# Kernel optimization log

Measured on AMD Instinct MI355X. Metric: run time of the kernel, lower is better.

## Reference

```python
import jax, jax.numpy as jnp
import numpy as np

TOP_K = 2

def setup_inputs() -> dict:
    key = jax.random.key(0)
    k1, k2, k3, k4 = jax.random.split(key, 4)
    T, H, I, E = 8192, 2048, 4096, 8
    s = 0.02
    return {
        "hidden_states": jax.random.normal(k1, (T, H), dtype=jnp.float32),
        "router_w": jax.random.normal(k2, (E, H), dtype=jnp.float32) * s,
        "ws": jax.random.normal(k3, (E, 2 * I, H), dtype=jnp.float32) * s,  # [gate; up]
        "w2s": jax.random.normal(k4, (E, H, I), dtype=jnp.float32) * s,
    }

def reference(hidden_states, router_w, ws, w2s):
    # Router gating: softmax over experts, top-k, NO renormalization
    logits = hidden_states @ router_w.T              # [T, E]
    probs = jax.nn.softmax(logits, axis=-1)
    topv, topi = jax.lax.top_k(probs, TOP_K)         # [T, K]
    T, E = probs.shape
    I = w2s.shape[2]
    # Dense routing-weight matrix [T, E]; top_k indices are unique per token
    w = jnp.zeros_like(probs).at[jnp.arange(T)[:, None], topi].set(topv)
    out = jnp.zeros_like(hidden_states)
    for e in range(E):  # fixed small expert loop; avoids [T,E,2I] blowup
        gate = hidden_states @ ws[e, :I].T           # [T, I]
        up = hidden_states @ ws[e, I:].T             # [T, I]
        h = jax.nn.silu(gate) * up                   # SwiGLU
        out = out + w[:, e:e + 1] * (h @ w2s[e].T)   # combine
    return out
```

## Files before the change

### kernel.cpp

```cpp
#include <hip/hip_runtime.h>
#include <cstdint>
#include <cstddef>

#define T_TOK 8192
#define HDIM  2048
#define IDIM  4096
#define NEXP  8
#define MAXT  72

typedef __bf16 bf16x8 __attribute__((ext_vector_type(8)));
typedef float  f32x4  __attribute__((ext_vector_type(4)));

#define BARRIER() __builtin_amdgcn_s_barrier()
#define VMW(n)    do { asm volatile("s_waitcnt vmcnt(" #n ")" ::: "memory"); } while (0)
#define PRIO1()   __builtin_amdgcn_s_setprio(1)
#define PRIO0()   __builtin_amdgcn_s_setprio(0)

__device__ __forceinline__ unsigned short f2bf(float f) {
    union { float f; unsigned u; } v; v.f = f;
    unsigned r = v.u + 0x7FFFu + ((v.u >> 16) & 1u);
    return (unsigned short)(r >> 16);
}

__device__ __forceinline__ void gload16(const void* g, void* l) {
    __builtin_amdgcn_global_load_lds((__attribute__((address_space(1))) void*)g,
                                     (__attribute__((address_space(3))) void*)l,
                                     16, 0, 0);
}

__global__ __launch_bounds__(256) void router_k(const float* __restrict__ hs,
                                                const float* __restrict__ rw,
                                                float* __restrict__ wgt,
                                                int* __restrict__ counts,
                                                int* __restrict__ lists,
                                                unsigned short* __restrict__ hs_bf) {
    int gid  = blockIdx.x * 256 + threadIdx.x;
    int tok  = gid >> 6;
    int lane = threadIdx.x & 63;
    const float* x = hs + (size_t)tok * HDIM;
    unsigned short* xb = hs_bf + (size_t)tok * HDIM;

    float acc[NEXP];
#pragma unroll
    for (int e = 0; e < NEXP; ++e) acc[e] = 0.f;
    for (int h = lane; h < HDIM; h += 64) {
        float xv = x[h];
        xb[h] = f2bf(xv);
#pragma unroll
        for (int e = 0; e < NEXP; ++e) acc[e] = fmaf(xv, rw[e * HDIM + h], acc[e]);
    }
#pragma unroll
    for (int off = 32; off > 0; off >>= 1) {
#pragma unroll
        for (int e = 0; e < NEXP; ++e) acc[e] += __shfl_xor(acc[e], off, 64);
    }
    if (lane == 0) {
        float m = acc[0];
#pragma unroll
        for (int e = 1; e < NEXP; ++e) m = fmaxf(m, acc[e]);
        float p[NEXP]; float s = 0.f;
#pragma unroll
        for (int e = 0; e < NEXP; ++e) { p[e] = expf(acc[e] - m); s += p[e]; }
        float inv = 1.f / s;
        int i1 = 0;
#pragma unroll
        for (int e = 1; e < NEXP; ++e) if (acc[e] > acc[i1]) i1 = e;
        int i2 = -1;
#pragma unroll
        for (int e = 0; e < NEXP; ++e) if (e != i1 && (i2 < 0 || acc[e] > acc[i2])) i2 = e;
#pragma unroll
        for (int e = 0; e < NEXP; ++e)
            wgt[(size_t)tok * NEXP + e] = (e == i1 || e == i2) ? p[e] * inv : 0.f;
        int p1 = atomicAdd(&counts[i1], 1);
        lists[i1 * T_TOK + p1] = tok;
        int p2 = atomicAdd(&counts[i2], 1);
        lists[i2 * T_TOK + p2] = (1 << 16) | tok;
    }
}

__global__ void plan_k(const int* __restrict__ counts, int* __restrict__ offs,
                       int* __restrict__ desc, int* __restrict__ ntiles) {
    if (threadIdx.x == 0 && blockIdx.x == 0) {
        int off = 0, n = 0;
        for (int e = 0; e < NEXP; ++e) {
            offs[e] = off;
            int nt = (counts[e] + 255) >> 8;
            for (int t = 0; t < nt; ++t) desc[n++] = (e << 16) | t;
            off += nt * 256;
        }
        *ntiles = n;
    }
}

__global__ __launch_bounds__(256) void cvt_k(const float* __restrict__ in,
                                             unsigned short* __restrict__ out, long n4) {
    long i      = (long)blockIdx.x * 256 + threadIdx.x;
    long stride = (long)gridDim.x * 256;
    const float4* in4 = (const float4*)in;
    ushort4* out4 = (ushort4*)out;
    for (long j = i; j < n4; j += stride) {
        float4 v = in4[j];
        ushort4 o;
        o.x = f2bf(v.x); o.y = f2bf(v.y); o.z = f2bf(v.z); o.w = f2bf(v.w);
        out4[j] = o;
    }
}

__global__ __launch_bounds__(512, 2) void gemm1_k(const unsigned short* __restrict__ A,
                                                  const unsigned short* __restrict__ Wall,
                                                  unsigned short* __restrict__ Hout,
                                                  const int* __restrict__ lists,
                                                  const int* __restrict__ counts,
                                                  const int* __restrict__ offs,
                                                  const int* __restrict__ desc,
                                                  const int* __restrict__ ntiles) {
    const int slot = blockIdx.y;
    if (slot >= *ntiles) return;
    const int dsc = desc[slot];
    const int e = dsc >> 16, tt = dsc & 0xFFFF;
    const int cnt = counts[e];
    const int t0 = tt * 256;
    const int* list = lists + e * T_TOK;
    const unsigned short* W = Wall + (size_t)e * 2 * IDIM * HDIM;
    const int hbase = offs[e];
    const int n0 = blockIdx.x * 128;

    extern __shared__ __align__(16) char lds[];

    const int tid  = threadIdx.x;
    const int lane = tid & 63;
    const int wid  = tid >> 6;
    const int wr   = wid >> 2;
    const int wc   = wid & 3;

    const int prow = tid >> 3;
    const int pcol = (tid & 7) * 16;
    const int lcol = (pcol ^ ((prow & 7) << 4)) >> 1;
    unsigned aoff[4];
#pragma unroll
    for (int i = 0; i < 4; ++i) {
        int g = t0 + i * 64 + prow;
        int tok = list[(g < cnt) ? g : t0] & 0xFFFF;
        aoff[i] = (unsigned)tok * HDIM + lcol;
    }
    unsigned goff[2], uoff[2];
#pragma unroll
    for (int i = 0; i < 2; ++i) {
        goff[i] = (unsigned)(n0 + i * 64 + prow) * HDIM + lcol;
        uoff[i] = (unsigned)(IDIM + n0 + i * 64 + prow) * HDIM + lcol;
    }
    const int dst = tid * 16;

#define SG_AH0(b, t) do { unsigned k0_ = (unsigned)((t) & 31) * 64;      \
    gload16(A + aoff[0] + k0_, lds + (b) * 32768 + dst);                 \
    gload16(A + aoff[1] + k0_, lds + (b) * 32768 + 8192 + dst); } while (0)
#define SG_AH1(b, t) do { unsigned k0_ = (unsigned)((t) & 31) * 64;      \
    gload16(A + aoff[2] + k0_, lds + (b) * 32768 + 16384 + dst);         \
    gload16(A + aoff[3] + k0_, lds + (b) * 32768 + 24576 + dst); } while (0)
#define SG_G(b, t) do { unsigned k0_ = (unsigned)((t) & 31) * 64;        \
    gload16(W + goff[0] + k0_, lds + 65536 + (b) * 16384 + dst);         \
    gload16(W + goff[1] + k0_, lds + 65536 + (b) * 16384 + 8192 + dst); } while (0)
#define SG_U(b, t) do { unsigned k0_ = (unsigned)((t) & 31) * 64;        \
    gload16(W + uoff[0] + k0_, lds + 98304 + (b) * 16384 + dst);         \
    gload16(W + uoff[1] + k0_, lds + 98304 + (b) * 16384 + 8192 + dst); } while (0)

    const int frd = (lane & 7) << 4;
    const int cb0 = (((lane >> 4) * 16)     ) ^ frd;
    const int cb1 = (((lane >> 4) * 16) | 64) ^ frd;
    const int arow = (wr * 64 + (lane & 15)) * 128;
    const int brow = (wc * 32 + (lane & 15)) * 128;

    f32x4 accg[8][2], accu[8][2];
#pragma unroll
    for (int mi = 0; mi < 8; ++mi)
#pragma unroll
        for (int ni = 0; ni < 2; ++ni) {
            accg[mi][ni] = (f32x4){0.f, 0.f, 0.f, 0.f};
            accu[mi][ni] = (f32x4){0.f, 0.f, 0.f, 0.f};
        }

    SG_AH0(0, 0); SG_G(0, 0); SG_U(0, 0); SG_AH1(0, 0);
    SG_AH0(1, 1); SG_G(1, 1);
    VMW(4);
    BARRIER();

    bf16x8 a0[2][4], a1[2][4], bg[2][2], bu[2][2];
    {
        const char* la = lds + arow;
        const char* lg = lds + 65536 + brow;
#pragma unroll
        for (int mi = 0; mi < 4; ++mi) {
            a0[0][mi] = *(const bf16x8*)(la + mi * 2048 + cb0);
            a0[1][mi] = *(const bf16x8*)(la + mi * 2048 + cb1);
        }
#pragma unroll
        for (int ni = 0; ni < 2; ++ni) {
            bg[0][ni] = *(const bf16x8*)(lg + ni * 2048 + cb0);
            bg[1][ni] = *(const bf16x8*)(lg + ni * 2048 + cb1);
        }
    }

    const int NT = HDIM / 64;
    for (int kt = 0; kt < NT; ++kt) {
        const int b  = kt & 1;
        const int bn = b ^ 1;
        const char* la  = lds + b * 32768 + arow;
        const char* lu  = lds + 98304 + b * 16384 + brow;
        const char* lan = lds + bn * 32768 + arow;
        const char* lgn = lds + 65536 + bn * 16384 + brow;

#pragma unroll
        for (int ni = 0; ni < 2; ++ni) {
            bu[0][ni] = *(const bf16x8*)(lu + ni * 2048 + cb0);
            bu[1][ni] = *(const bf16x8*)(lu + ni * 2048 + cb1);
        }
        SG_AH1(bn, kt + 1);
        PRIO1();
#pragma unroll
        for (int ks = 0; ks < 2; ++ks)
#pragma unroll
            for (int mi = 0; mi < 4; ++mi)
#pragma unroll
                for (int ni = 0; ni < 2; ++ni)
                    accg[mi][ni] = __builtin_amdgcn_mfma_f32_16x16x32_bf16(a0[ks][mi], bg[ks][ni], accg[mi][ni], 0, 0, 0);
        PRIO0(); BARRIER();

#pragma unroll
        for (int mi = 0; mi < 4; ++mi) {
            a1[0][mi] = *(const bf16x8*)(la + 16384 + mi * 2048 + cb0);
            a1[1][mi] = *(const bf16x8*)(la + 16384 + mi * 2048 + cb1);
        }
        SG_U(bn, kt + 1);
        PRIO1();
#pragma unroll
        for (int ks = 0; ks < 2; ++ks)
#pragma unroll
            for (int mi = 0; mi < 4; ++mi)
#pragma unroll
                for (int ni = 0; ni < 2; ++ni)
                    accu[mi][ni] = __builtin_amdgcn_mfma_f32_16x16x32_bf16(a0[ks][mi], bu[ks][ni], accu[mi][ni], 0, 0, 0);
        PRIO0(); BARRIER();

        SG_AH0(b, kt + 2);
        PRIO1();
#pragma unroll
        for (int ks = 0; ks < 2; ++ks)
#pragma unroll
            for (int mi = 0; mi < 4; ++mi)
#pragma unroll
                for (int ni = 0; ni < 2; ++ni)
                    accg[mi + 4][ni] = __builtin_amdgcn_mfma_f32_16x16x32_bf16(a1[ks][mi], bg[ks][ni], accg[mi + 4][ni], 0, 0, 0);
        PRIO0(); BARRIER();

        SG_G(b, kt + 2);
        VMW(4);
        BARRIER();
#pragma unroll
        for (int mi = 0; mi < 4; ++mi) {
            a0[0][mi] = *(const bf16x8*)(lan + mi * 2048 + cb0);
            a0[1][mi] = *(const bf16x8*)(lan + mi * 2048 + cb1);
        }
#pragma unroll
        for (int ni = 0; ni < 2; ++ni) {
            bg[0][ni] = *(const bf16x8*)(lgn + ni * 2048 + cb0);
            bg[1][ni] = *(const bf16x8*)(lgn + ni * 2048 + cb1);
        }
        PRIO1();
#pragma unroll
        for (int ks = 0; ks < 2; ++ks)
#pragma unroll
            for (int mi = 0; mi < 4; ++mi)
#pragma unroll
                for (int ni = 0; ni < 2; ++ni)
                    accu[mi + 4][ni] = __builtin_amdgcn_mfma_f32_16x16x32_bf16(a1[ks][mi], bu[ks][ni], accu[mi + 4][ni], 0, 0, 0);
        PRIO0();
        BARRIER();
    }
    VMW(0);
#undef SG_AH0
#undef SG_AH1
#undef SG_G
#undef SG_U

#pragma unroll
    for (int mi = 0; mi < 8; ++mi)
#pragma unroll
        for (int ni = 0; ni < 2; ++ni)
#pragma unroll
            for (int j = 0; j < 4; ++j) {
                int qr = mi >> 2, m = mi & 3;
                int row = hbase + t0 + qr * 128 + wr * 64 + m * 16 + ((lane >> 4) << 2) + j;
                int col = n0 + wc * 32 + ni * 16 + (lane & 15);
                float g = accg[mi][ni][j], u = accu[mi][ni][j];
                float hv = (g / (1.f + expf(-g))) * u;
                Hout[(size_t)row * IDIM + col] = f2bf(hv);
            }
}

__global__ __launch_bounds__(512, 2) void gemm2_k(const unsigned short* __restrict__ Ah,
                                                  const unsigned short* __restrict__ Ball,
                                                  const float* __restrict__ wgt,
                                                  float* __restrict__ outP,
                                                  const int* __restrict__ lists,
                                                  const int* __restrict__ counts,
                                                  const int* __restrict__ offs,
                                                  const int* __restrict__ desc,
                                                  const int* __restrict__ ntiles) {
    const int slot = blockIdx.y;
    if (slot >= *ntiles) return;
    const int dsc = desc[slot];
    const int e = dsc >> 16, tt = dsc & 0xFFFF;
    const int cnt = counts[e];
    const int t0 = tt * 256;
    const int* list = lists + e * T_TOK;
    const unsigned short* B = Ball + (size_t)e * HDIM * IDIM;
    const int hbase = offs[e];
    const int n0 = blockIdx.x * 256;

    extern __shared__ __align__(16) char lds[];

    const int tid  = threadIdx.x;
    const int lane = tid & 63;
    const int wid  = tid >> 6;
    const int wr   = wid >> 2;
    const int wc   = wid & 3;

    const int prow = tid >> 3;
    const int pcol = (tid & 7) * 16;
    const int lcol = (pcol ^ ((prow & 7) << 4)) >> 1;
    unsigned aoff[4], boff[4];
#pragma unroll
    for (int i = 0; i < 4; ++i) {
        aoff[i] = (unsigned)(hbase + t0 + i * 64 + prow) * IDIM + lcol;
        boff[i] = (unsigned)(n0 + i * 64 + prow) * IDIM + lcol;
    }
    const int dst = tid * 16;

#define SG_AH0(b, t) do { unsigned k0_ = (unsigned)((t) & 63) * 64;       \
    gload16(Ah + aoff[0] + k0_, lds + (b) * 32768 + dst);                 \
    gload16(Ah + aoff[1] + k0_, lds + (b) * 32768 + 8192 + dst); } while (0)
#define SG_AH1(b, t) do { unsigned k0_ = (unsigned)((t) & 63) * 64;       \
    gload16(Ah + aoff[2] + k0_, lds + (b) * 32768 + 16384 + dst);         \
    gload16(Ah + aoff[3] + k0_, lds + (b) * 32768 + 24576 + dst); } while (0)
#define SG_BH0(b, t) do { unsigned k0_ = (unsigned)((t) & 63) * 64;       \
    gload16(B + boff[0] + k0_, lds + 65536 + (b) * 32768 + dst);          \
    gload16(B + boff[1] + k0_, lds + 65536 + (b) * 32768 + 8192 + dst); } while (0)
#define SG_BH1(b, t) do { unsigned k0_ = (unsigned)((t) & 63) * 64;       \
    gload16(B + boff[2] + k0_, lds + 65536 + (b) * 32768 + 16384 + dst);  \
    gload16(B + boff[3] + k0_, lds + 65536 + (b) * 32768 + 24576 + dst); } while (0)

    const int frd = (lane & 7) << 4;
    const int cb0 = (((lane >> 4) * 16)     ) ^ frd;
    const int cb1 = (((lane >> 4) * 16) | 64) ^ frd;
    const int arow = (wr * 64 + (lane & 15)) * 128;
    const int brow = (wc * 64 + (lane & 15)) * 128;

    f32x4 acc[8][4];
#pragma unroll
    for (int mi = 0; mi < 8; ++mi)
#pragma unroll
        for (int ni = 0; ni < 4; ++ni) acc[mi][ni] = (f32x4){0.f, 0.f, 0.f, 0.f};

    SG_AH0(0, 0); SG_BH0(0, 0); SG_AH1(0, 0); SG_BH1(0, 0);
    SG_AH0(1, 1); SG_BH0(1, 1);
    VMW(4);
    BARRIER();

    bf16x8 a0[2][4], a1[2][4], b01[2][2], b23[2][2];
    {
        const char* la = lds + arow;
        const char* lb = lds + 65536 + brow;
#pragma unroll
        for (int mi = 0; mi < 4; ++mi) {
            a0[0][mi] = *(const bf16x8*)(la + mi * 2048 + cb0);
            a0[1][mi] = *(const bf16x8*)(la + mi * 2048 + cb1);
        }
#pragma unroll
        for (int ni = 0; ni < 2; ++ni) {
            b01[0][ni] = *(const bf16x8*)(lb + ni * 2048 + cb0);
            b01[1][ni] = *(const bf16x8*)(lb + ni * 2048 + cb1);
        }
    }

    const int NT = IDIM / 64;
    for (int kt = 0; kt < NT; ++kt) {
        const int b  = kt & 1;
        const int bn = b ^ 1;
        const char* la  = lds + b * 32768 + arow;
        const char* lb  = lds + 65536 + b * 32768 + brow;
        const char* lan = lds + bn * 32768 + arow;
        const char* lbn = lds + 65536 + bn * 32768 + brow;

#pragma unroll
        for (int ni = 0; ni < 2; ++ni) {
            b23[0][ni] = *(const bf16x8*)(lb + (ni + 2) * 2048 + cb0);
            b23[1][ni] = *(const bf16x8*)(lb + (ni + 2) * 2048 + cb1);
        }
        SG_AH1(bn, kt + 1);
        PRIO1();
#pragma unroll
        for (int ks = 0; ks < 2; ++ks)
#pragma unroll
            for (int mi = 0; mi < 4; ++mi)
#pragma unroll
                for (int ni = 0; ni < 2; ++ni)
                    acc[mi][ni] = __builtin_amdgcn_mfma_f32_16x16x32_bf16(a0[ks][mi], b01[ks][ni], acc[mi][ni], 0, 0, 0);
        PRIO0(); BARRIER();

#pragma unroll
        for (int mi = 0; mi < 4; ++mi) {
            a1[0][mi] = *(const bf16x8*)(la + 16384 + mi * 2048 + cb0);
            a1[1][mi] = *(const bf16x8*)(la + 16384 + mi * 2048 + cb1);
        }
        SG_BH1(bn, kt + 1);
        PRIO1();
#pragma unroll
        for (int ks = 0; ks < 2; ++ks)
#pragma unroll
            for (int mi = 0; mi < 4; ++mi)
#pragma unroll
                for (int ni = 0; ni < 2; ++ni)
                    acc[mi][ni + 2] = __builtin_amdgcn_mfma_f32_16x16x32_bf16(a0[ks][mi], b23[ks][ni], acc[mi][ni + 2], 0, 0, 0);
        PRIO0(); BARRIER();

        SG_AH0(b, kt + 2);
        PRIO1();
#pragma unroll
        for (int ks = 0; ks < 2; ++ks)
#pragma unroll
            for (int mi = 0; mi < 4; ++mi)
#pragma unroll
                for (int ni = 0; ni < 2; ++ni)
                    acc[mi + 4][ni] = __builtin_amdgcn_mfma_f32_16x16x32_bf16(a1[ks][mi], b01[ks][ni], acc[mi + 4][ni], 0, 0, 0);
        PRIO0(); BARRIER();

        SG_BH0(b, kt + 2);
        VMW(4);
        BARRIER();
#pragma unroll
        for (int mi = 0; mi < 4; ++mi) {
            a0[0][mi] = *(const bf16x8*)(lan + mi * 2048 + cb0);
            a0[1][mi] = *(const bf16x8*)(lan + mi * 2048 + cb1);
        }
#pragma unroll
        for (int ni = 0; ni < 2; ++ni) {
            b01[0][ni] = *(const bf16x8*)(lbn + ni * 2048 + cb0);
            b01[1][ni] = *(const bf16x8*)(lbn + ni * 2048 + cb1);
        }
        PRIO1();
#pragma unroll
        for (int ks = 0; ks < 2; ++ks)
#pragma unroll
            for (int mi = 0; mi < 4; ++mi)
#pragma unroll
                for (int ni = 0; ni < 2; ++ni)
                    acc[mi + 4][ni + 2] = __builtin_amdgcn_mfma_f32_16x16x32_bf16(a1[ks][mi], b23[ks][ni], acc[mi + 4][ni + 2], 0, 0, 0);
        PRIO0();
        BARRIER();
    }
    VMW(0);
#undef SG_AH0
#undef SG_AH1
#undef SG_BH0
#undef SG_BH1

#pragma unroll
    for (int mi = 0; mi < 8; ++mi) {
        int qr = mi >> 2, m = mi & 3;
#pragma unroll
        for (int j = 0; j < 4; ++j) {
            int g = t0 + qr * 128 + wr * 64 + m * 16 + ((lane >> 4) << 2) + j;
            if (g < cnt) {
                int ent = list[g];
                int tok = ent & 0xFFFF;
                int sl  = ent >> 16;
                float w = wgt[(size_t)tok * NEXP + e];
                float* o = outP + (size_t)sl * T_TOK * HDIM + (size_t)tok * HDIM;
#pragma unroll
                for (int ni = 0; ni < 4; ++ni) {
                    int col = n0 + wc * 64 + ni * 16 + (lane & 15);
                    o[col] = w * acc[mi][ni][j];
                }
            }
        }
    }
}

__global__ __launch_bounds__(256) void combine_k(const float* __restrict__ p0,
                                                 const float* __restrict__ p1,
                                                 float* __restrict__ out, long n4) {
    long i      = (long)blockIdx.x * 256 + threadIdx.x;
    long stride = (long)gridDim.x * 256;
    const float4* a4 = (const float4*)p0;
    const float4* b4 = (const float4*)p1;
    float4* o4 = (float4*)out;
    for (long j = i; j < n4; j += stride) {
        float4 a = a4[j], b = b4[j];
        o4[j] = make_float4(a.x + b.x, a.y + b.y, a.z + b.z, a.w + b.w);
    }
}

extern "C" void kernel_launch(void* const* d_in, const int* in_sizes, int n_in,
                              void* d_out, int out_size, void* d_ws, size_t ws_size,
                              hipStream_t stream) {
    const float* hs  = (const float*)d_in[0];
    const float* rw  = (const float*)d_in[1];
    const float* ws  = (const float*)d_in[2];
    const float* w2s = (const float*)d_in[3];
    float* out = (float*)d_out;

    char* wsp = (char*)d_ws;
    unsigned short* hs_bf = (unsigned short*)(wsp);
    unsigned short* w_bf  = (unsigned short*)(wsp + 33554432ULL);
    unsigned short* w2_bf = (unsigned short*)(wsp + 301989888ULL);
    unsigned short* h_bf  = (unsigned short*)(wsp + 436207616ULL);
    float*          outP  = (float*)(wsp + 587202560ULL);
    float*          wgt   = (float*)(wsp + 721420288ULL);
    int*            counts = (int*)(wsp + 721682432ULL);
    int*            offs   = (int*)(wsp + 721682560ULL);
    int*            lists  = (int*)(wsp + 721682688ULL);
    int*            desc   = (int*)(wsp + 721944832ULL);
    int*            ntiles = (int*)(wsp + 721945344ULL);

    hipMemsetAsync(counts, 0, NEXP * sizeof(int), stream);
    cvt_k<<<4096, 256, 0, stream>>>(ws, w_bf, (long)NEXP * 2 * IDIM * HDIM / 4);
    cvt_k<<<4096, 256, 0, stream>>>(w2s, w2_bf, (long)NEXP * HDIM * IDIM / 4);
    router_k<<<(T_TOK * 64) / 256, 256, 0, stream>>>(hs, rw, wgt, counts, lists, hs_bf);
    plan_k<<<1, 64, 0, stream>>>(counts, offs, desc, ntiles);

    gemm1_k<<<dim3(IDIM / 128, MAXT), 512, 131072, stream>>>(
        hs_bf, w_bf, h_bf, lists, counts, offs, desc, ntiles);
    gemm2_k<<<dim3(HDIM / 256, MAXT), 512, 131072, stream>>>(
        h_bf, w2_bf, wgt, outP, lists, counts, offs, desc, ntiles);
    combine_k<<<2048, 256, 0, stream>>>(outP, outP + (size_t)T_TOK * HDIM, out,
                                        (long)T_TOK * HDIM / 4);
}
```

Before: 1.349 ms.

## Split the K dimension of the down-projection GEMM in two, reducing partials in combine

gemm2_k gains a blockIdx.z dimension: each z-slice handles half of the 4096-long reduction (32 of the 64 k-tiles). Each slice writes its own pair of per-slot partial planes, so there are now four fp32 partial planes. combine_k sums all four planes into the output. This doubles the block count of the second GEMM to fill the GPU better and soften the tail wave. In exchange it writes and then reads two extra full-size fp32 planes and needs a larger workspace.

```diff
diff --git a/kernel.cpp b/kernel.cpp
--- a/kernel.cpp
+++ b/kernel.cpp
@@ -300,7 +300,7 @@
 __global__ __launch_bounds__(512, 2) void gemm2_k(const unsigned short* __restrict__ Ah,
                                                   const unsigned short* __restrict__ Ball,
                                                   const float* __restrict__ wgt,
-                                                  float* __restrict__ outP,
+                                                  float* __restrict__ outP4,
                                                   const int* __restrict__ lists,
                                                   const int* __restrict__ counts,
                                                   const int* __restrict__ offs,
@@ -316,6 +316,8 @@
     const unsigned short* B = Ball + (size_t)e * HDIM * IDIM;
     const int hbase = offs[e];
     const int n0 = blockIdx.x * 256;
+    const int kz = blockIdx.z;
+    const int kt0 = kz * 32;
 
     extern __shared__ __align__(16) char lds[];
 
@@ -361,8 +363,8 @@
 #pragma unroll
         for (int ni = 0; ni < 4; ++ni) acc[mi][ni] = (f32x4){0.f, 0.f, 0.f, 0.f};
 
-    SG_AH0(0, 0); SG_BH0(0, 0); SG_AH1(0, 0); SG_BH1(0, 0);
-    SG_AH0(1, 1); SG_BH0(1, 1);
+    SG_AH0(0, kt0); SG_BH0(0, kt0); SG_AH1(0, kt0); SG_BH1(0, kt0);
+    SG_AH0(1, kt0 + 1); SG_BH0(1, kt0 + 1);
     VMW(4);
     BARRIER();
 
@@ -382,8 +384,7 @@
         }
     }
 
-    const int NT = IDIM / 64;
-    for (int kt = 0; kt < NT; ++kt) {
+    for (int kt = kt0; kt < kt0 + 32; ++kt) {
         const int b  = kt & 1;
         const int bn = b ^ 1;
         const char* la  = lds + b * 32768 + arow;
@@ -475,7 +476,7 @@
                 int tok = ent & 0xFFFF;
                 int sl  = ent >> 16;
                 float w = wgt[(size_t)tok * NEXP + e];
-                float* o = outP + (size_t)sl * T_TOK * HDIM + (size_t)tok * HDIM;
+                float* o = outP4 + (size_t)(kz * 2 + sl) * T_TOK * HDIM + (size_t)tok * HDIM;
 #pragma unroll
                 for (int ni = 0; ni < 4; ++ni) {
                     int col = n0 + wc * 64 + ni * 16 + (lane & 15);
@@ -486,17 +487,20 @@
     }
 }
 
-__global__ __launch_bounds__(256) void combine_k(const float* __restrict__ p0,
-                                                 const float* __restrict__ p1,
-                                                 float* __restrict__ out, long n4) {
+__global__ __launch_bounds__(256) void combine_k(const float* __restrict__ pl, float* __restrict__ out,
+                                                 long n4) {
     long i      = (long)blockIdx.x * 256 + threadIdx.x;
     long stride = (long)gridDim.x * 256;
-    const float4* a4 = (const float4*)p0;
-    const float4* b4 = (const float4*)p1;
+    const long plane4 = (long)T_TOK * HDIM / 4;
+    const float4* p0 = (const float4*)pl;
+    const float4* p1 = p0 + plane4;
+    const float4* p2 = p1 + plane4;
+    const float4* p3 = p2 + plane4;
     float4* o4 = (float4*)out;
     for (long j = i; j < n4; j += stride) {
-        float4 a = a4[j], b = b4[j];
-        o4[j] = make_float4(a.x + b.x, a.y + b.y, a.z + b.z, a.w + b.w);
+        float4 a = p0[j], b = p1[j], c = p2[j], d = p3[j];
+        o4[j] = make_float4((a.x + b.x) + (c.x + d.x), (a.y + b.y) + (c.y + d.y),
+                            (a.z + b.z) + (c.z + d.z), (a.w + b.w) + (c.w + d.w));
     }
 }
 
@@ -514,13 +518,13 @@
     unsigned short* w_bf  = (unsigned short*)(wsp + 33554432ULL);
     unsigned short* w2_bf = (unsigned short*)(wsp + 301989888ULL);
     unsigned short* h_bf  = (unsigned short*)(wsp + 436207616ULL);
-    float*          outP  = (float*)(wsp + 587202560ULL);
-    float*          wgt   = (float*)(wsp + 721420288ULL);
-    int*            counts = (int*)(wsp + 721682432ULL);
-    int*            offs   = (int*)(wsp + 721682560ULL);
-    int*            lists  = (int*)(wsp + 721682688ULL);
-    int*            desc   = (int*)(wsp + 721944832ULL);
-    int*            ntiles = (int*)(wsp + 721945344ULL);
+    float*          outP4 = (float*)(wsp + 587202560ULL);
+    float*          wgt   = (float*)(wsp + 855638016ULL);
+    int*            counts = (int*)(wsp + 855900160ULL);
+    int*            offs   = (int*)(wsp + 855900288ULL);
+    int*            lists  = (int*)(wsp + 855900416ULL);
+    int*            desc   = (int*)(wsp + 856162560ULL);
+    int*            ntiles = (int*)(wsp + 856163072ULL);
 
     hipMemsetAsync(counts, 0, NEXP * sizeof(int), stream);
     cvt_k<<<4096, 256, 0, stream>>>(ws, w_bf, (long)NEXP * 2 * IDIM * HDIM / 4);
@@ -530,8 +534,7 @@
 
     gemm1_k<<<dim3(IDIM / 128, MAXT), 512, 131072, stream>>>(
         hs_bf, w_bf, h_bf, lists, counts, offs, desc, ntiles);
-    gemm2_k<<<dim3(HDIM / 256, MAXT), 512, 131072, stream>>>(
-        h_bf, w2_bf, wgt, outP, lists, counts, offs, desc, ntiles);
-    combine_k<<<2048, 256, 0, stream>>>(outP, outP + (size_t)T_TOK * HDIM, out,
-                                        (long)T_TOK * HDIM / 4);
-}
+    gemm2_k<<<dim3(HDIM / 256, MAXT, 2), 512, 131072, stream>>>(
+        h_bf, w2_bf, wgt, outP4, lists, counts, offs, desc, ntiles);
+    combine_k<<<2048, 256, 0, stream>>>(outP4, out, (long)T_TOK * HDIM / 4);
+}
```

New measurement: 1.379 ms. 1.02x slower.

## Fuse fp32-to-bf16 weight conversion into gemm1 loads, dropping the cvt pass

Applied to the files above, without the earlier changes.

Removes the separate conversion kernel for the gate/up weights. gemm1 now reads the fp32 weights directly into registers, converts them to bf16 in-kernel and writes them to LDS, replacing the async global-to-LDS copies for B. This saves a 512MB read and 256MB write pass over the weights. In exchange, each gemm1 tile re-reads fp32 weights (twice the bytes of bf16) across many token tiles. The change also adds register pressure and extra waits/barriers in the pipelined main loop.

```diff
diff --git a/kernel.cpp b/kernel.cpp
--- a/kernel.cpp
+++ b/kernel.cpp
@@ -12,6 +12,7 @@
 typedef float  f32x4  __attribute__((ext_vector_type(4)));
 
 #define BARRIER() __builtin_amdgcn_s_barrier()
+#define LGKM0()   do { asm volatile("s_waitcnt lgkmcnt(0)" ::: "memory"); } while (0)
 #define VMW(n)    do { asm volatile("s_waitcnt vmcnt(" #n ")" ::: "memory"); } while (0)
 #define PRIO1()   __builtin_amdgcn_s_setprio(1)
 #define PRIO0()   __builtin_amdgcn_s_setprio(0)
@@ -107,7 +108,7 @@
 }
 
 __global__ __launch_bounds__(512, 2) void gemm1_k(const unsigned short* __restrict__ A,
-                                                  const unsigned short* __restrict__ Wall,
+                                                  const float* __restrict__ Wf,
                                                   unsigned short* __restrict__ Hout,
                                                   const int* __restrict__ lists,
                                                   const int* __restrict__ counts,
@@ -121,7 +122,7 @@
     const int cnt = counts[e];
     const int t0 = tt * 256;
     const int* list = lists + e * T_TOK;
-    const unsigned short* W = Wall + (size_t)e * 2 * IDIM * HDIM;
+    const float* W = Wf + (size_t)e * 2 * IDIM * HDIM;
     const int hbase = offs[e];
     const int n0 = blockIdx.x * 128;
 
@@ -157,12 +158,26 @@
 #define SG_AH1(b, t) do { unsigned k0_ = (unsigned)((t) & 31) * 64;      \
     gload16(A + aoff[2] + k0_, lds + (b) * 32768 + 16384 + dst);         \
     gload16(A + aoff[3] + k0_, lds + (b) * 32768 + 24576 + dst); } while (0)
-#define SG_G(b, t) do { unsigned k0_ = (unsigned)((t) & 31) * 64;        \
-    gload16(W + goff[0] + k0_, lds + 65536 + (b) * 16384 + dst);         \
-    gload16(W + goff[1] + k0_, lds + 65536 + (b) * 16384 + 8192 + dst); } while (0)
-#define SG_U(b, t) do { unsigned k0_ = (unsigned)((t) & 31) * 64;        \
-    gload16(W + uoff[0] + k0_, lds + 98304 + (b) * 16384 + dst);         \
-    gload16(W + uoff[1] + k0_, lds + 98304 + (b) * 16384 + 8192 + dst); } while (0)
+#define LDF_G(t) do { unsigned k0_ = (unsigned)((t) & 31) * 64;          \
+    gw[0] = *(const f32x4*)(W + goff[0] + k0_);                          \
+    gw[1] = *(const f32x4*)(W + goff[0] + k0_ + 4);                      \
+    gw[2] = *(const f32x4*)(W + goff[1] + k0_);                          \
+    gw[3] = *(const f32x4*)(W + goff[1] + k0_ + 4); } while (0)
+#define LDF_U(t) do { unsigned k0_ = (unsigned)((t) & 31) * 64;          \
+    uw[0] = *(const f32x4*)(W + uoff[0] + k0_);                          \
+    uw[1] = *(const f32x4*)(W + uoff[0] + k0_ + 4);                      \
+    uw[2] = *(const f32x4*)(W + uoff[1] + k0_);                          \
+    uw[3] = *(const f32x4*)(W + uoff[1] + k0_ + 4); } while (0)
+#define CVW(base, R) do {                                                \
+    bf16x8 v0_, v1_;                                                     \
+    _Pragma("unroll") for (int i_ = 0; i_ < 4; ++i_) {                   \
+        v0_[i_]     = (__bf16)R[0][i_];                                  \
+        v0_[i_ + 4] = (__bf16)R[1][i_];                                  \
+        v1_[i_]     = (__bf16)R[2][i_];                                  \
+        v1_[i_ + 4] = (__bf16)R[3][i_];                                  \
+    }                                                                    \
+    *(bf16x8*)(lds + (base) + dst) = v0_;                                \
+    *(bf16x8*)(lds + (base) + 8192 + dst) = v1_; } while (0)
 
     const int frd = (lane & 7) << 4;
     const int cb0 = (((lane >> 4) * 16)     ) ^ frd;
@@ -179,9 +194,14 @@
             accu[mi][ni] = (f32x4){0.f, 0.f, 0.f, 0.f};
         }
 
-    SG_AH0(0, 0); SG_G(0, 0); SG_U(0, 0); SG_AH1(0, 0);
-    SG_AH0(1, 1); SG_G(1, 1);
-    VMW(4);
+    f32x4 gw[4], uw[4];
+    LDF_G(0); CVW(65536, gw);
+    LDF_U(0); CVW(98304, uw);
+    LDF_G(1); CVW(65536 + 16384, gw);
+    LDF_U(1); CVW(98304 + 16384, uw);
+    SG_AH0(0, 0); SG_AH1(0, 0); SG_AH0(1, 1);
+    VMW(0);
+    LGKM0();
     BARRIER();
 
     bf16x8 a0[2][4], a1[2][4], bg[2][2], bu[2][2];
@@ -214,6 +234,7 @@
             bu[0][ni] = *(const bf16x8*)(lu + ni * 2048 + cb0);
             bu[1][ni] = *(const bf16x8*)(lu + ni * 2048 + cb1);
         }
+        LDF_G(kt + 2);
         SG_AH1(bn, kt + 1);
         PRIO1();
 #pragma unroll
@@ -230,7 +251,7 @@
             a1[0][mi] = *(const bf16x8*)(la + 16384 + mi * 2048 + cb0);
             a1[1][mi] = *(const bf16x8*)(la + 16384 + mi * 2048 + cb1);
         }
-        SG_U(bn, kt + 1);
+        LDF_U(kt + 2);
         PRIO1();
 #pragma unroll
         for (int ks = 0; ks < 2; ++ks)
@@ -241,7 +262,9 @@
                     accu[mi][ni] = __builtin_amdgcn_mfma_f32_16x16x32_bf16(a0[ks][mi], bu[ks][ni], accu[mi][ni], 0, 0, 0);
         PRIO0(); BARRIER();
 
+        VMW(6);
         SG_AH0(b, kt + 2);
+        CVW(65536 + b * 16384, gw);
         PRIO1();
 #pragma unroll
         for (int ks = 0; ks < 2; ++ks)
@@ -250,10 +273,13 @@
 #pragma unroll
                 for (int ni = 0; ni < 2; ++ni)
                     accg[mi + 4][ni] = __builtin_amdgcn_mfma_f32_16x16x32_bf16(a1[ks][mi], bg[ks][ni], accg[mi + 4][ni], 0, 0, 0);
-        PRIO0(); BARRIER();
-
-        SG_G(b, kt + 2);
-        VMW(4);
+        PRIO0();
+        LGKM0();
+        BARRIER();
+
+        VMW(2);
+        CVW(98304 + b * 16384, uw);
+        LGKM0();
         BARRIER();
 #pragma unroll
         for (int mi = 0; mi < 4; ++mi) {
@@ -279,8 +305,9 @@
     VMW(0);
 #undef SG_AH0
 #undef SG_AH1
-#undef SG_G
-#undef SG_U
+#undef LDF_G
+#undef LDF_U
+#undef CVW
 
 #pragma unroll
     for (int mi = 0; mi < 8; ++mi)
@@ -511,7 +538,6 @@
 
     char* wsp = (char*)d_ws;
     unsigned short* hs_bf = (unsigned short*)(wsp);
-    unsigned short* w_bf  = (unsigned short*)(wsp + 33554432ULL);
     unsigned short* w2_bf = (unsigned short*)(wsp + 301989888ULL);
     unsigned short* h_bf  = (unsigned short*)(wsp + 436207616ULL);
     float*          outP  = (float*)(wsp + 587202560ULL);
@@ -523,13 +549,12 @@
     int*            ntiles = (int*)(wsp + 721945344ULL);
 
     hipMemsetAsync(counts, 0, NEXP * sizeof(int), stream);
-    cvt_k<<<4096, 256, 0, stream>>>(ws, w_bf, (long)NEXP * 2 * IDIM * HDIM / 4);
     cvt_k<<<4096, 256, 0, stream>>>(w2s, w2_bf, (long)NEXP * HDIM * IDIM / 4);
     router_k<<<(T_TOK * 64) / 256, 256, 0, stream>>>(hs, rw, wgt, counts, lists, hs_bf);
     plan_k<<<1, 64, 0, stream>>>(counts, offs, desc, ntiles);
 
     gemm1_k<<<dim3(IDIM / 128, MAXT), 512, 131072, stream>>>(
-        hs_bf, w_bf, h_bf, lists, counts, offs, desc, ntiles);
+        hs_bf, ws, h_bf, lists, counts, offs, desc, ntiles);
     gemm2_k<<<dim3(HDIM / 256, MAXT), 512, 131072, stream>>>(
         h_bf, w2_bf, wgt, outP, lists, counts, offs, desc, ntiles);
     combine_k<<<2048, 256, 0, stream>>>(outP, outP + (size_t)T_TOK * HDIM, out,
```

Result: slower. 2.316 ms (+71.7%).

## Shrink gemm1 K-tile to 32 with simpler double-buffered pipeline and 64KB LDS

Applied to the files above, without the earlier changes.

Restructures the gate/up GEMM kernel to use a K-step of 32 instead of 64, with one combined stage-load per iteration and static 64KB shared memory instead of 128KB dynamic. The intricate four-phase interleaved schedule is replaced by a plain double buffer that waits for all loads at the end of each iteration. The smaller LDS footprint is meant to allow more resident blocks per CU. In exchange it doubles the iteration count and barrier frequency and loses the fine-grained load/compute overlap.

```diff
diff --git a/kernel.cpp b/kernel.cpp
--- a/kernel.cpp
+++ b/kernel.cpp
@@ -125,7 +125,7 @@
     const int hbase = offs[e];
     const int n0 = blockIdx.x * 128;
 
-    extern __shared__ __align__(16) char lds[];
+    __shared__ __align__(16) char lds[65536];
 
     const int tid  = threadIdx.x;
     const int lane = tid & 63;
@@ -133,42 +133,28 @@
     const int wr   = wid >> 2;
     const int wc   = wid & 3;
 
-    const int prow = tid >> 3;
-    const int pcol = (tid & 7) * 16;
-    const int lcol = (pcol ^ ((prow & 7) << 4)) >> 1;
-    unsigned aoff[4];
-#pragma unroll
-    for (int i = 0; i < 4; ++i) {
-        int g = t0 + i * 64 + prow;
-        int tok = list[(g < cnt) ? g : t0] & 0xFFFF;
-        aoff[i] = (unsigned)tok * HDIM + lcol;
-    }
-    unsigned goff[2], uoff[2];
-#pragma unroll
-    for (int i = 0; i < 2; ++i) {
-        goff[i] = (unsigned)(n0 + i * 64 + prow) * HDIM + lcol;
-        uoff[i] = (unsigned)(IDIM + n0 + i * 64 + prow) * HDIM + lcol;
-    }
+    const int prow = tid >> 2;
+    const int pcol = (tid & 3) * 16;
+    const int lcol = (pcol ^ (((prow >> 1) & 3) << 4)) >> 1;
+    const int g0 = t0 + prow, g1 = t0 + 128 + prow;
+    const unsigned tok0 = (unsigned)(list[(g0 < cnt) ? g0 : t0] & 0xFFFF);
+    const unsigned tok1 = (unsigned)(list[(g1 < cnt) ? g1 : t0] & 0xFFFF);
+    const unsigned aoff0 = tok0 * HDIM + lcol;
+    const unsigned aoff1 = tok1 * HDIM + lcol;
+    const unsigned goff  = (unsigned)(n0 + prow) * HDIM + lcol;
+    const unsigned uoff  = (unsigned)(IDIM + n0 + prow) * HDIM + lcol;
     const int dst = tid * 16;
 
-#define SG_AH0(b, t) do { unsigned k0_ = (unsigned)((t) & 31) * 64;      \
-    gload16(A + aoff[0] + k0_, lds + (b) * 32768 + dst);                 \
-    gload16(A + aoff[1] + k0_, lds + (b) * 32768 + 8192 + dst); } while (0)
-#define SG_AH1(b, t) do { unsigned k0_ = (unsigned)((t) & 31) * 64;      \
-    gload16(A + aoff[2] + k0_, lds + (b) * 32768 + 16384 + dst);         \
-    gload16(A + aoff[3] + k0_, lds + (b) * 32768 + 24576 + dst); } while (0)
-#define SG_G(b, t) do { unsigned k0_ = (unsigned)((t) & 31) * 64;        \
-    gload16(W + goff[0] + k0_, lds + 65536 + (b) * 16384 + dst);         \
-    gload16(W + goff[1] + k0_, lds + 65536 + (b) * 16384 + 8192 + dst); } while (0)
-#define SG_U(b, t) do { unsigned k0_ = (unsigned)((t) & 31) * 64;        \
-    gload16(W + uoff[0] + k0_, lds + 98304 + (b) * 16384 + dst);         \
-    gload16(W + uoff[1] + k0_, lds + 98304 + (b) * 16384 + 8192 + dst); } while (0)
-
-    const int frd = (lane & 7) << 4;
-    const int cb0 = (((lane >> 4) * 16)     ) ^ frd;
-    const int cb1 = (((lane >> 4) * 16) | 64) ^ frd;
-    const int arow = (wr * 64 + (lane & 15)) * 128;
-    const int brow = (wc * 32 + (lane & 15)) * 128;
+#define SG(b, t) do { unsigned k0_ = (unsigned)((t) & 63) * 32;       \
+    gload16(A + aoff0 + k0_, lds + (b) * 16384 + dst);                \
+    gload16(A + aoff1 + k0_, lds + (b) * 16384 + 8192 + dst);         \
+    gload16(W + goff + k0_, lds + 32768 + (b) * 8192 + dst);          \
+    gload16(W + uoff + k0_, lds + 49152 + (b) * 8192 + dst); } while (0)
+
+    const int frd = (((lane & 15) >> 1) & 3) << 4;
+    const int cb  = ((lane >> 4) << 4) ^ frd;
+    const int arow = (wr * 64 + (lane & 15)) * 64;
+    const int brow = (wc * 32 + (lane & 15)) * 64;
 
     f32x4 accg[8][2], accu[8][2];
 #pragma unroll
@@ -179,108 +165,64 @@
             accu[mi][ni] = (f32x4){0.f, 0.f, 0.f, 0.f};
         }
 
-    SG_AH0(0, 0); SG_G(0, 0); SG_U(0, 0); SG_AH1(0, 0);
-    SG_AH0(1, 1); SG_G(1, 1);
-    VMW(4);
+    SG(0, 0);
+    VMW(0);
     BARRIER();
 
-    bf16x8 a0[2][4], a1[2][4], bg[2][2], bu[2][2];
+    bf16x8 a0[4], a1[4], bg[2], bu[2];
     {
         const char* la = lds + arow;
-        const char* lg = lds + 65536 + brow;
-#pragma unroll
-        for (int mi = 0; mi < 4; ++mi) {
-            a0[0][mi] = *(const bf16x8*)(la + mi * 2048 + cb0);
-            a0[1][mi] = *(const bf16x8*)(la + mi * 2048 + cb1);
-        }
+#pragma unroll
+        for (int m = 0; m < 4; ++m) a0[m] = *(const bf16x8*)(la + m * 1024 + cb);
 #pragma unroll
         for (int ni = 0; ni < 2; ++ni) {
-            bg[0][ni] = *(const bf16x8*)(lg + ni * 2048 + cb0);
-            bg[1][ni] = *(const bf16x8*)(lg + ni * 2048 + cb1);
-        }
-    }
-
-    const int NT = HDIM / 64;
+            bg[ni] = *(const bf16x8*)(lds + 32768 + brow + ni * 1024 + cb);
+            bu[ni] = *(const bf16x8*)(lds + 49152 + brow + ni * 1024 + cb);
+        }
+    }
+
+    const int NT = HDIM / 32;
     for (int kt = 0; kt < NT; ++kt) {
         const int b  = kt & 1;
         const int bn = b ^ 1;
-        const char* la  = lds + b * 32768 + arow;
-        const char* lu  = lds + 98304 + b * 16384 + brow;
-        const char* lan = lds + bn * 32768 + arow;
-        const char* lgn = lds + 65536 + bn * 16384 + brow;
-
-#pragma unroll
-        for (int ni = 0; ni < 2; ++ni) {
-            bu[0][ni] = *(const bf16x8*)(lu + ni * 2048 + cb0);
-            bu[1][ni] = *(const bf16x8*)(lu + ni * 2048 + cb1);
-        }
-        SG_AH1(bn, kt + 1);
-        PRIO1();
-#pragma unroll
-        for (int ks = 0; ks < 2; ++ks)
-#pragma unroll
-            for (int mi = 0; mi < 4; ++mi)
-#pragma unroll
-                for (int ni = 0; ni < 2; ++ni)
-                    accg[mi][ni] = __builtin_amdgcn_mfma_f32_16x16x32_bf16(a0[ks][mi], bg[ks][ni], accg[mi][ni], 0, 0, 0);
-        PRIO0(); BARRIER();
-
-#pragma unroll
-        for (int mi = 0; mi < 4; ++mi) {
-            a1[0][mi] = *(const bf16x8*)(la + 16384 + mi * 2048 + cb0);
-            a1[1][mi] = *(const bf16x8*)(la + 16384 + mi * 2048 + cb1);
-        }
-        SG_U(bn, kt + 1);
-        PRIO1();
-#pragma unroll
-        for (int ks = 0; ks < 2; ++ks)
-#pragma unroll
-            for (int mi = 0; mi < 4; ++mi)
-#pragma unroll
-                for (int ni = 0; ni < 2; ++ni)
-                    accu[mi][ni] = __builtin_amdgcn_mfma_f32_16x16x32_bf16(a0[ks][mi], bu[ks][ni], accu[mi][ni], 0, 0, 0);
-        PRIO0(); BARRIER();
-
-        SG_AH0(b, kt + 2);
-        PRIO1();
-#pragma unroll
-        for (int ks = 0; ks < 2; ++ks)
-#pragma unroll
-            for (int mi = 0; mi < 4; ++mi)
-#pragma unroll
-                for (int ni = 0; ni < 2; ++ni)
-                    accg[mi + 4][ni] = __builtin_amdgcn_mfma_f32_16x16x32_bf16(a1[ks][mi], bg[ks][ni], accg[mi + 4][ni], 0, 0, 0);
-        PRIO0(); BARRIER();
-
-        SG_G(b, kt + 2);
-        VMW(4);
+        const char* la = lds + b * 16384 + arow;
+
+#pragma unroll
+        for (int m = 0; m < 4; ++m) a1[m] = *(const bf16x8*)(la + 8192 + m * 1024 + cb);
+        SG(bn, kt + 1);
+        PRIO1();
+#pragma unroll
+        for (int m = 0; m < 4; ++m)
+#pragma unroll
+            for (int ni = 0; ni < 2; ++ni) {
+                accg[m][ni] = __builtin_amdgcn_mfma_f32_16x16x32_bf16(a0[m], bg[ni], accg[m][ni], 0, 0, 0);
+                accu[m][ni] = __builtin_amdgcn_mfma_f32_16x16x32_bf16(a0[m], bu[ni], accu[m][ni], 0, 0, 0);
+            }
+        PRIO0();
+
+        PRIO1();
+#pragma unroll
+        for (int m = 0; m < 4; ++m)
+#pragma unroll
+            for (int ni = 0; ni < 2; ++ni) {
+                accg[m + 4][ni] = __builtin_amdgcn_mfma_f32_16x16x32_bf16(a1[m], bg[ni], accg[m + 4][ni], 0, 0, 0);
+                accu[m + 4][ni] = __builtin_amdgcn_mfma_f32_16x16x32_bf16(a1[m], bu[ni], accu[m + 4][ni], 0, 0, 0);
+            }
+        PRIO0();
+        VMW(0);
         BARRIER();
-#pragma unroll
-        for (int mi = 0; mi < 4; ++mi) {
-            a0[0][mi] = *(const bf16x8*)(lan + mi * 2048 + cb0);
-            a0[1][mi] = *(const bf16x8*)(lan + mi * 2048 + cb1);
-        }
-#pragma unroll
-        for (int ni = 0; ni < 2; ++ni) {
-            bg[0][ni] = *(const bf16x8*)(lgn + ni * 2048 + cb0);
-            bg[1][ni] = *(const bf16x8*)(lgn + ni * 2048 + cb1);
-        }
-        PRIO1();
-#pragma unroll
-        for (int ks = 0; ks < 2; ++ks)
-#pragma unroll
-            for (int mi = 0; mi < 4; ++mi)
-#pragma unroll
-                for (int ni = 0; ni < 2; ++ni)
-                    accu[mi + 4][ni] = __builtin_amdgcn_mfma_f32_16x16x32_bf16(a1[ks][mi], bu[ks][ni], accu[mi + 4][ni], 0, 0, 0);
-        PRIO0();
-        BARRIER();
-    }
-    VMW(0);
-#undef SG_AH0
-#undef SG_AH1
-#undef SG_G
-#undef SG_U
+        {
+            const char* lan = lds + bn * 16384 + arow;
+#pragma unroll
+            for (int m = 0; m < 4; ++m) a0[m] = *(const bf16x8*)(lan + m * 1024 + cb);
+#pragma unroll
+            for (int ni = 0; ni < 2; ++ni) {
+                bg[ni] = *(const bf16x8*)(lds + 32768 + bn * 8192 + brow + ni * 1024 + cb);
+                bu[ni] = *(const bf16x8*)(lds + 49152 + bn * 8192 + brow + ni * 1024 + cb);
+            }
+        }
+    }
+#undef SG
 
 #pragma unroll
     for (int mi = 0; mi < 8; ++mi)
@@ -528,7 +470,7 @@
     router_k<<<(T_TOK * 64) / 256, 256, 0, stream>>>(hs, rw, wgt, counts, lists, hs_bf);
     plan_k<<<1, 64, 0, stream>>>(counts, offs, desc, ntiles);
 
-    gemm1_k<<<dim3(IDIM / 128, MAXT), 512, 131072, stream>>>(
+    gemm1_k<<<dim3(IDIM / 128, MAXT), 512, 0, stream>>>(
         hs_bf, w_bf, h_bf, lists, counts, offs, desc, ntiles);
     gemm2_k<<<dim3(HDIM / 256, MAXT), 512, 131072, stream>>>(
         h_bf, w2_bf, wgt, outP, lists, counts, offs, desc, ntiles);
```

Measured after the change: 1.481 ms. +9.8%, slower.
